# Optimization experiments

Measured on AMD Instinct MI355X. Metric: run time of the kernel, lower is better.

The kernel has to match this reference:

```python
import jax, jax.numpy as jnp
import numpy as np

FEAT_DIM = 384
HEAD_DIM = 32
N_HEADS = FEAT_DIM // HEAD_DIM
MAX_SEQ_LEN = 64
SIZE = 8  # sqrt(max_seq_len)


def _get_relative_position_index(height, width):
    coords_h = np.arange(height)
    coords_w = np.arange(width)
    coords = np.stack(np.meshgrid(coords_h, coords_w, indexing='ij'))
    coords_flat = coords.reshape(coords.shape[0], -1)
    relative_coords = coords_flat[:, :, None] - coords_flat[:, None, :]
    relative_coords = relative_coords.transpose(1, 2, 0)
    rh = relative_coords[:, :, 0] + (height - 1)
    rw = relative_coords[:, :, 1] + (width - 1)
    return jnp.asarray(rh * (2 * width - 1) + rw, dtype=jnp.int32)  # [P, P]


def setup_inputs() -> dict:
    key = jax.random.key(0)
    ks = jax.random.split(key, 6)
    B, G, P, D = 32, 64, MAX_SEQ_LEN, FEAT_DIM
    x = jax.random.normal(ks[0], (B, G, P, D), dtype=jnp.float32)
    qkv_w = jax.random.normal(ks[1], (D, 3 * D), dtype=jnp.float32) * (1.0 / np.sqrt(D))
    qkv_b = jnp.zeros((3 * D,), dtype=jnp.float32)
    merge_w = jax.random.normal(ks[2], (D, D), dtype=jnp.float32) * (1.0 / np.sqrt(D))
    merge_b = jnp.zeros((D,), dtype=jnp.float32)
    n_bias = (2 * SIZE - 1) * (2 * SIZE - 1)  # 225
    bias_table = jax.random.truncated_normal(ks[3], -2.0, 2.0, (n_bias, N_HEADS), dtype=jnp.float32) * 0.02
    rel_index = _get_relative_position_index(SIZE, SIZE)
    return {"x": x, "qkv_w": qkv_w, "qkv_b": qkv_b, "merge_w": merge_w,
            "merge_b": merge_b, "bias_table": bias_table, "rel_index": rel_index}


def reference(x, qkv_w, qkv_b, merge_w, merge_b, bias_table, rel_index):
    B, G, P, D = x.shape
    H, DH = N_HEADS, HEAD_DIM
    scale = 1.0 / np.sqrt(D)  # NOTE: module scales by feat_dim**-0.5, not head_dim
    qkv = x @ qkv_w + qkv_b  # [B,G,P,3D]
    q, k, v = jnp.split(qkv, 3, axis=-1)
    q = q.reshape(B, G, P, H, DH).transpose(0, 1, 3, 2, 4)  # [B,G,H,P,DH]
    k = k.reshape(B, G, P, H, DH).transpose(0, 1, 3, 2, 4)
    v = v.reshape(B, G, P, H, DH).transpose(0, 1, 3, 2, 4)
    scores = jnp.einsum('bghid,bghjd->bghij', q, k * scale)  # [B,G,H,P,P]
    pos_bias = bias_table[rel_index.reshape(-1)].reshape(P, P, H)
    pos_bias = pos_bias.transpose(2, 0, 1)[None, None]  # [1,1,H,P,P]
    attn = jax.nn.softmax(scores + pos_bias, axis=-1)
    out = jnp.einsum('bghij,bghjd->bghid', attn, v)  # [B,G,H,P,DH]
    out = out.transpose(0, 1, 3, 2, 4).reshape(B, G, P, D)
    return out @ merge_w + merge_b
```

## Files before the change

kernel.cpp:

```cpp
#include <hip/hip_runtime.h>
#include <hip/hip_bf16.h>
#include <cstdint>
#include <cstddef>


typedef __bf16 bf16_t;
typedef __bf16 bf16x8 __attribute__((ext_vector_type(8)));
typedef float  f32x4  __attribute__((ext_vector_type(4)));

#define MFMA16(A, B, C) __builtin_amdgcn_mfma_f32_16x16x32_bf16((A), (B), (C), 0, 0, 0)

#define SCALE  0.051031036307982884f
#define LOG2E  1.4426950408889634f

#define BAR()  do { asm volatile("s_waitcnt lgkmcnt(0)" ::: "memory"); \
                    __builtin_amdgcn_s_barrier(); } while (0)


__global__ void prep_kernel(const float* __restrict__ qkv_w,
                            const float* __restrict__ qkv_b,
                            const float* __restrict__ merge_w,
                            const float* __restrict__ bias_table,
                            const int*   __restrict__ rel_index,
                            bf16_t* __restrict__ qkv_wT,
                            bf16_t* __restrict__ merge_wT,
                            bf16_t* __restrict__ biasx,
                            float*  __restrict__ qkvb_s) {
  int idx = blockIdx.x * 256 + threadIdx.x;
  if (idx < 1152 * 384) {
    int n = idx / 384, k = idx - n * 384;
    float v = qkv_w[k * 1152 + n];
    if (n >= 384 && n < 768) v *= SCALE;
    qkv_wT[idx] = (bf16_t)v;
    return;
  }
  int i2 = idx - 1152 * 384;
  if (i2 < 384 * 384) {
    int n = i2 / 384, k = i2 - n * 384;
    merge_wT[i2] = (bf16_t)merge_w[k * 384 + n];
    return;
  }
  int i3 = i2 - 384 * 384;
  if (i3 < 12 * 64 * 64) {
    int h = i3 / 4096, r = i3 - h * 4096;
    biasx[i3] = (bf16_t)bias_table[rel_index[r] * 12 + h];
    return;
  }
  int i4 = i3 - 12 * 64 * 64;
  if (i4 < 1152) {
    float v = qkv_b[i4];
    if (i4 >= 384 && i4 < 768) v *= SCALE;
    qkvb_s[i4] = v;
  }
}

__device__ inline float bflo(unsigned u) {
  union { unsigned x; float f; } v; v.x = u << 16; return v.f;
}
__device__ inline float bfhi(unsigned u) {
  union { unsigned x; float f; } v; v.x = u & 0xffff0000u; return v.f;
}

__global__ void __launch_bounds__(768, 6)
fused_qkv_attn(const float*  __restrict__ x,
               const bf16_t* __restrict__ wT,
               const float*  __restrict__ qbias,
               const bf16_t* __restrict__ biasx,
               bf16_t* __restrict__ attn) {
  extern __shared__ char smem_raw[];
  bf16_t* lds = (bf16_t*)smem_raw;
  bf16_t* xs  = lds;
  bf16_t* qs  = lds;
  bf16_t* ks  = lds + 8192;
  bf16_t* vts = lds + 16384;
  bf16_t* ps  = lds + 24576;

  const int tid  = threadIdx.x;
  const int lane = tid & 63;
  const int w    = tid >> 6;
  const int c    = lane & 15;
  const int g    = lane >> 4;
  const int cx   = c & 7;

  const int xcd  = blockIdx.x & 7;
  const int slot = blockIdx.x >> 3;
  const int pass = slot % 3;
  const int bg   = (slot / 3) * 8 + xcd;

  const f32x4 zf = {0.f, 0.f, 0.f, 0.f};

  {
    const float4* xg = (const float4*)(x + (size_t)bg * 24576);
#pragma unroll
    for (int it = 0; it < 4; ++it) {
      int hc  = tid + it * 768;
      int row = hc / 48;
      int ch  = hc - row * 48;
      float4 v0 = xg[hc * 2];
      float4 v1 = xg[hc * 2 + 1];
      union { bf16_t b[8]; bf16x8 v; } pk;
      pk.b[0] = (bf16_t)v0.x; pk.b[1] = (bf16_t)v0.y;
      pk.b[2] = (bf16_t)v0.z; pk.b[3] = (bf16_t)v0.w;
      pk.b[4] = (bf16_t)v1.x; pk.b[5] = (bf16_t)v1.y;
      pk.b[6] = (bf16_t)v1.z; pk.b[7] = (bf16_t)v1.w;
      *(bf16x8*)(xs + row * 384 + ((ch ^ (row & 7)) << 3)) = pk.v;
    }
  }
  BAR();

  f32x4 acc[2][4];
#pragma unroll
  for (int t = 0; t < 2; ++t)
#pragma unroll
    for (int mt = 0; mt < 4; ++mt) acc[t][mt] = zf;

  int nrow[2];
  const int kind = (w * 2) >> 3;
  int hlv[2], c16v[2];
  const bf16_t* wp[2];
  float bv[2];
#pragma unroll
  for (int t = 0; t < 2; ++t) {
    int tau  = w * 2 + t;
    int u    = tau & 7;
    hlv[t]   = u >> 1;
    c16v[t]  = u & 1;
    nrow[t]  = kind * 384 + (pass * 4 + hlv[t]) * 32 + c16v[t] * 16;
    wp[t]    = wT + (size_t)(nrow[t] + c) * 384 + g * 8;
    bv[t]    = qbias[nrow[t] + c];
  }
  bf16x8 bc[2], bn[2];
#pragma unroll
  for (int t = 0; t < 2; ++t) bc[t] = *(const bf16x8*)(wp[t]);

#pragma unroll
  for (int k = 0; k < 12; ++k) {
    if (k < 11) {
#pragma unroll
      for (int t = 0; t < 2; ++t) bn[t] = *(const bf16x8*)(wp[t] + (k + 1) * 32);
    }
    int chv = (((4 * k + g) ^ cx) << 3);
#pragma unroll
    for (int mt = 0; mt < 4; ++mt) {
      bf16x8 a = *(const bf16x8*)(xs + (mt * 16 + c) * 384 + chv);
#pragma unroll
      for (int t = 0; t < 2; ++t)
        acc[t][mt] = MFMA16(a, bc[t], acc[t][mt]);
    }
#pragma unroll
    for (int t = 0; t < 2; ++t) bc[t] = bn[t];
  }

  BAR();

#pragma unroll
  for (int t = 0; t < 2; ++t) {
    int hl = hlv[t], c16 = c16v[t];
    if (kind == 2) {
      int d = c16 * 16 + c;
      bf16_t* vbase = vts + hl * 2048 + d * 64;
#pragma unroll
      for (int mt = 0; mt < 4; ++mt) {
        union { bf16_t b[4]; uint2 u2; } pk;
#pragma unroll
        for (int r = 0; r < 4; ++r) pk.b[r] = (bf16_t)(acc[t][mt][r] + bv[t]);
        int chunk = (2 * mt + (g >> 1)) ^ cx;
        *(uint2*)(vbase + chunk * 8 + (g & 1) * 4) = pk.u2;
      }
    } else {
      int f  = c16 * 16 + c;
      int fc = f >> 3;
      int fl = f & 7;
      bf16_t* dst = (kind == 0 ? qs : ks) + hl * 2048;
#pragma unroll
      for (int mt = 0; mt < 4; ++mt)
#pragma unroll
        for (int r = 0; r < 4; ++r)
          dst[(mt * 16 + g * 4 + r) * 32 + ((fc ^ g) << 3) + fl] =
              (bf16_t)(acc[t][mt][r] + bv[t]);
    }
  }
  BAR();

  if (w < 8) {
    const int hl = w >> 1, ih = w & 1;
    const int h  = pass * 4 + hl;
    const int rsw = (c >> 2) & 3;

    const bf16_t* bp = biasx + h * 4096;
    bf16x8 ka[4], va[2][2];
#pragma unroll
    for (int mt = 0; mt < 4; ++mt)
      ka[mt] = *(const bf16x8*)(ks + hl * 2048 + (mt * 16 + c) * 32 +
                                ((g ^ rsw) << 3));
#pragma unroll
    for (int m2 = 0; m2 < 2; ++m2)
#pragma unroll
      for (int kt = 0; kt < 2; ++kt)
        va[m2][kt] = *(const bf16x8*)(vts + hl * 2048 + (m2 * 16 + c) * 64 +
                                      (((4 * kt + g) ^ cx) << 3));

    bf16_t* psw = ps + w * 1024;

#pragma unroll
    for (int nt = 0; nt < 2; ++nt) {
      int i = ih * 32 + nt * 16 + c;
      bf16x8 qf = *(const bf16x8*)(qs + hl * 2048 + i * 32 + ((g ^ rsw) << 3));

      f32x4 sacc[4];
#pragma unroll
      for (int mt = 0; mt < 4; ++mt) sacc[mt] = zf;
#pragma unroll
      for (int mt = 0; mt < 4; ++mt)
        sacc[mt] = MFMA16(ka[mt], qf, sacc[mt]);

      float l = 0.f;
#pragma unroll
      for (int mt = 0; mt < 4; ++mt) {
        uint2 bb = *(const uint2*)(bp + i * 64 + mt * 16 + g * 4);
        float p0 = exp2f((sacc[mt][0] + bflo(bb.x)) * LOG2E);
        float p1 = exp2f((sacc[mt][1] + bfhi(bb.x)) * LOG2E);
        float p2 = exp2f((sacc[mt][2] + bflo(bb.y)) * LOG2E);
        float p3 = exp2f((sacc[mt][3] + bfhi(bb.y)) * LOG2E);
        l += (p0 + p1) + (p2 + p3);
        union { bf16_t b[4]; uint2 u2; } pk;
        pk.b[0] = (bf16_t)p0; pk.b[1] = (bf16_t)p1;
        pk.b[2] = (bf16_t)p2; pk.b[3] = (bf16_t)p3;
        int chunk = (2 * mt + (g >> 1)) ^ cx;
        *(uint2*)(psw + c * 64 + chunk * 8 + (g & 1) * 4) = pk.u2;
      }
      bf16x8 pb[2];
#pragma unroll
      for (int kt = 0; kt < 2; ++kt)
        pb[kt] = *(const bf16x8*)(psw + c * 64 + (((4 * kt + g) ^ cx) << 3));
      f32x4 oacc[2];
#pragma unroll
      for (int m2 = 0; m2 < 2; ++m2) oacc[m2] = zf;
#pragma unroll
      for (int m2 = 0; m2 < 2; ++m2)
#pragma unroll
        for (int kt = 0; kt < 2; ++kt)
          oacc[m2] = MFMA16(va[m2][kt], pb[kt], oacc[m2]);

      l += __shfl_xor(l, 16);
      l += __shfl_xor(l, 32);
      float inv = 1.0f / l;

      int row = bg * 64 + i;
#pragma unroll
      for (int m2 = 0; m2 < 2; ++m2) {
        union { bf16_t b[4]; uint2 u2; } pk;
#pragma unroll
        for (int r = 0; r < 4; ++r) pk.b[r] = (bf16_t)(oacc[m2][r] * inv);
        *(uint2*)(attn + (size_t)row * 384 + h * 32 + m2 * 16 + g * 4) = pk.u2;
      }
    }
  }
}

#define XS 408
__global__ void __launch_bounds__(512)
merge_gemm(const bf16_t* __restrict__ attn,
           const bf16_t* __restrict__ mwT,
           const float*  __restrict__ mb,
           float* __restrict__ out) {
  __shared__ bf16_t as[64 * XS];
  const int tid = threadIdx.x, blk = blockIdx.x;
  const int lane = tid & 63, w = tid >> 6, c = lane & 15, g = lane >> 4;

  {
    const int4* ag = (const int4*)(attn + (size_t)blk * (64 * 384));
#pragma unroll
    for (int it = 0; it < 6; ++it) {
      int idx = tid + it * 512;
      int row = idx / 48;
      int col = (idx - row * 48) * 8;
      *(int4*)(as + row * XS + col) = ag[idx];
    }
  }
  __syncthreads();

  const f32x4 zf = {0.f, 0.f, 0.f, 0.f};
  f32x4 acc[3][4];
#pragma unroll
  for (int t = 0; t < 3; ++t)
#pragma unroll
    for (int mt = 0; mt < 4; ++mt) acc[t][mt] = zf;

  const int n0 = w * 48;
  const bf16_t* wp[3];
#pragma unroll
  for (int t = 0; t < 3; ++t) wp[t] = mwT + (size_t)(n0 + t * 16 + c) * 384 + g * 8;
  bf16x8 bc[3], bn[3];
#pragma unroll
  for (int t = 0; t < 3; ++t) bc[t] = *(const bf16x8*)(wp[t]);
#pragma unroll
  for (int k = 0; k < 12; ++k) {
    if (k < 11) {
#pragma unroll
      for (int t = 0; t < 3; ++t) bn[t] = *(const bf16x8*)(wp[t] + (k + 1) * 32);
    }
    bf16x8 a[4];
#pragma unroll
    for (int mt = 0; mt < 4; ++mt)
      a[mt] = *(const bf16x8*)(as + (mt * 16 + c) * XS + k * 32 + g * 8);
#pragma unroll
    for (int t = 0; t < 3; ++t)
#pragma unroll
      for (int mt = 0; mt < 4; ++mt)
        acc[t][mt] = MFMA16(a[mt], bc[t], acc[t][mt]);
#pragma unroll
    for (int t = 0; t < 3; ++t) bc[t] = bn[t];
  }

#pragma unroll
  for (int t = 0; t < 3; ++t) {
    float bias = mb[n0 + t * 16 + c];
#pragma unroll
    for (int mt = 0; mt < 4; ++mt)
#pragma unroll
      for (int r = 0; r < 4; ++r)
        out[(size_t)(blk * 64 + mt * 16 + g * 4 + r) * 384 + n0 + t * 16 + c] =
            acc[t][mt][r] + bias;
  }
}

extern "C" void kernel_launch(void* const* d_in, const int* in_sizes, int n_in,
                              void* d_out, int out_size, void* d_ws, size_t ws_size,
                              hipStream_t stream) {
  const float* x          = (const float*)d_in[0];
  const float* qkv_w      = (const float*)d_in[1];
  const float* qkv_b      = (const float*)d_in[2];
  const float* merge_w    = (const float*)d_in[3];
  const float* merge_b    = (const float*)d_in[4];
  const float* bias_table = (const float*)d_in[5];
  const int*   rel_index  = (const int*)d_in[6];
  float*       out        = (float*)d_out;

  const size_t OFF_QKVWT = 0;
  const size_t OFF_MWT   = 884736;
  const size_t OFF_BIAS  = OFF_MWT + 294912;
  const size_t OFF_QB    = OFF_BIAS + 98304;
  const size_t OFF_ATTN  = OFF_QB + 4608;
  const size_t NEED      = OFF_ATTN + (size_t)100663296;
  if (ws_size < NEED) return;

  char* ws = (char*)d_ws;
  bf16_t* qkv_wT  = (bf16_t*)(ws + OFF_QKVWT);
  bf16_t* mwT     = (bf16_t*)(ws + OFF_MWT);
  bf16_t* biasx   = (bf16_t*)(ws + OFF_BIAS);
  float*  qkvb_s  = (float*)(ws + OFF_QB);
  bf16_t* attnbuf = (bf16_t*)(ws + OFF_ATTN);

  prep_kernel<<<2501, 256, 0, stream>>>(qkv_w, qkv_b, merge_w, bias_table,
                                        rel_index, qkv_wT, mwT, biasx, qkvb_s);

  hipFuncSetAttribute(reinterpret_cast<const void*>(fused_qkv_attn),
                      hipFuncAttributeMaxDynamicSharedMemorySize, 65536);
  fused_qkv_attn<<<6144, 768, 65536, stream>>>(x, qkv_wT, qkvb_s, biasx, attnbuf);

  merge_gemm<<<2048, 512, 0, stream>>>(attnbuf, mwT, merge_b, out);
}
```

Baseline: 409.1 us.

## Fuse QKV, attention, and merge projection into one kernel per group

Result: slower. 677.2 us (+65.5%).

```diff
diff --git a/kernel.cpp b/kernel.cpp
--- a/kernel.cpp
+++ b/kernel.cpp
@@ -62,18 +62,21 @@
 }
 
 __global__ void __launch_bounds__(768, 6)
-fused_qkv_attn(const float*  __restrict__ x,
-               const bf16_t* __restrict__ wT,
-               const float*  __restrict__ qbias,
-               const bf16_t* __restrict__ biasx,
-               bf16_t* __restrict__ attn) {
+mega_kernel(const float*  __restrict__ x,
+            const bf16_t* __restrict__ wT,
+            const float*  __restrict__ qbias,
+            const bf16_t* __restrict__ biasx,
+            const bf16_t* __restrict__ mwT,
+            const float*  __restrict__ mb,
+            float* __restrict__ out) {
   extern __shared__ char smem_raw[];
   bf16_t* lds = (bf16_t*)smem_raw;
   bf16_t* xs  = lds;
-  bf16_t* qs  = lds;
-  bf16_t* ks  = lds + 8192;
-  bf16_t* vts = lds + 16384;
-  bf16_t* ps  = lds + 24576;
+  bf16_t* qs  = lds + 24576;
+  bf16_t* ks  = lds + 32768;
+  bf16_t* vts = lds + 40960;
+  bf16_t* ao  = lds + 49152;
+  bf16_t* ps  = qs;
 
   const int tid  = threadIdx.x;
   const int lane = tid & 63;
@@ -81,11 +84,7 @@
   const int c    = lane & 15;
   const int g    = lane >> 4;
   const int cx   = c & 7;
-
-  const int xcd  = blockIdx.x & 7;
-  const int slot = blockIdx.x >> 3;
-  const int pass = slot % 3;
-  const int bg   = (slot / 3) * 8 + xcd;
+  const int bg   = blockIdx.x;
 
   const f32x4 zf = {0.f, 0.f, 0.f, 0.f};
 
@@ -108,220 +107,210 @@
   }
   BAR();
 
-  f32x4 acc[2][4];
-#pragma unroll
-  for (int t = 0; t < 2; ++t)
-#pragma unroll
-    for (int mt = 0; mt < 4; ++mt) acc[t][mt] = zf;
-
-  int nrow[2];
-  const int kind = (w * 2) >> 3;
-  int hlv[2], c16v[2];
-  const bf16_t* wp[2];
-  float bv[2];
-#pragma unroll
-  for (int t = 0; t < 2; ++t) {
-    int tau  = w * 2 + t;
-    int u    = tau & 7;
-    hlv[t]   = u >> 1;
-    c16v[t]  = u & 1;
-    nrow[t]  = kind * 384 + (pass * 4 + hlv[t]) * 32 + c16v[t] * 16;
-    wp[t]    = wT + (size_t)(nrow[t] + c) * 384 + g * 8;
-    bv[t]    = qbias[nrow[t] + c];
-  }
-  bf16x8 bc[2], bn[2];
-#pragma unroll
-  for (int t = 0; t < 2; ++t) bc[t] = *(const bf16x8*)(wp[t]);
-
-#pragma unroll
-  for (int k = 0; k < 12; ++k) {
-    if (k < 11) {
-#pragma unroll
-      for (int t = 0; t < 2; ++t) bn[t] = *(const bf16x8*)(wp[t] + (k + 1) * 32);
-    }
-    int chv = (((4 * k + g) ^ cx) << 3);
-#pragma unroll
-    for (int mt = 0; mt < 4; ++mt) {
-      bf16x8 a = *(const bf16x8*)(xs + (mt * 16 + c) * 384 + chv);
-#pragma unroll
-      for (int t = 0; t < 2; ++t)
-        acc[t][mt] = MFMA16(a, bc[t], acc[t][mt]);
-    }
-#pragma unroll
-    for (int t = 0; t < 2; ++t) bc[t] = bn[t];
-  }
-
-  BAR();
-
-#pragma unroll
-  for (int t = 0; t < 2; ++t) {
-    int hl = hlv[t], c16 = c16v[t];
-    if (kind == 2) {
-      int d = c16 * 16 + c;
-      bf16_t* vbase = vts + hl * 2048 + d * 64;
+#pragma unroll 1
+  for (int pass = 0; pass < 3; ++pass) {
+    f32x4 acc[2][4];
+#pragma unroll
+    for (int t = 0; t < 2; ++t)
+#pragma unroll
+      for (int mt = 0; mt < 4; ++mt) acc[t][mt] = zf;
+
+    const int kind = (w * 2) >> 3;
+    int nrow[2], hlv[2], c16v[2];
+    const bf16_t* wp[2];
+    float bv[2];
+#pragma unroll
+    for (int t = 0; t < 2; ++t) {
+      int tau  = w * 2 + t;
+      int u    = tau & 7;
+      hlv[t]   = u >> 1;
+      c16v[t]  = u & 1;
+      nrow[t]  = kind * 384 + (pass * 4 + hlv[t]) * 32 + c16v[t] * 16;
+      wp[t]    = wT + (size_t)(nrow[t] + c) * 384 + g * 8;
+      bv[t]    = qbias[nrow[t] + c];
+    }
+    bf16x8 bc[2], bn[2];
+#pragma unroll
+    for (int t = 0; t < 2; ++t) bc[t] = *(const bf16x8*)(wp[t]);
+
+#pragma unroll
+    for (int k = 0; k < 12; ++k) {
+      if (k < 11) {
+#pragma unroll
+        for (int t = 0; t < 2; ++t) bn[t] = *(const bf16x8*)(wp[t] + (k + 1) * 32);
+      }
+      int chv = (((4 * k + g) ^ cx) << 3);
 #pragma unroll
       for (int mt = 0; mt < 4; ++mt) {
-        union { bf16_t b[4]; uint2 u2; } pk;
-#pragma unroll
-        for (int r = 0; r < 4; ++r) pk.b[r] = (bf16_t)(acc[t][mt][r] + bv[t]);
-        int chunk = (2 * mt + (g >> 1)) ^ cx;
-        *(uint2*)(vbase + chunk * 8 + (g & 1) * 4) = pk.u2;
-      }
-    } else {
-      int f  = c16 * 16 + c;
-      int fc = f >> 3;
-      int fl = f & 7;
-      bf16_t* dst = (kind == 0 ? qs : ks) + hl * 2048;
-#pragma unroll
-      for (int mt = 0; mt < 4; ++mt)
-#pragma unroll
-        for (int r = 0; r < 4; ++r)
-          dst[(mt * 16 + g * 4 + r) * 32 + ((fc ^ g) << 3) + fl] =
-              (bf16_t)(acc[t][mt][r] + bv[t]);
-    }
-  }
-  BAR();
-
-  if (w < 8) {
+        bf16x8 a = *(const bf16x8*)(xs + (mt * 16 + c) * 384 + chv);
+#pragma unroll
+        for (int t = 0; t < 2; ++t)
+          acc[t][mt] = MFMA16(a, bc[t], acc[t][mt]);
+      }
+#pragma unroll
+      for (int t = 0; t < 2; ++t) bc[t] = bn[t];
+    }
+
+    BAR();
+
+#pragma unroll
+    for (int t = 0; t < 2; ++t) {
+      int hl = hlv[t], c16 = c16v[t];
+      if (kind == 2) {
+        int d = c16 * 16 + c;
+        bf16_t* vbase = vts + hl * 2048 + d * 64;
+#pragma unroll
+        for (int mt = 0; mt < 4; ++mt) {
+          union { bf16_t b[4]; uint2 u2; } pk;
+#pragma unroll
+          for (int r = 0; r < 4; ++r) pk.b[r] = (bf16_t)(acc[t][mt][r] + bv[t]);
+          int chunk = (2 * mt + (g >> 1)) ^ cx;
+          *(uint2*)(vbase + chunk * 8 + (g & 1) * 4) = pk.u2;
+        }
+      } else {
+        int f  = c16 * 16 + c;
+        int fc = f >> 3;
+        int fl = f & 7;
+        bf16_t* dst = (kind == 0 ? qs : ks) + hl * 2048;
+#pragma unroll
+        for (int mt = 0; mt < 4; ++mt)
+#pragma unroll
+          for (int r = 0; r < 4; ++r)
+            dst[(mt * 16 + g * 4 + r) * 32 + ((fc ^ g) << 3) + fl] =
+                (bf16_t)(acc[t][mt][r] + bv[t]);
+      }
+    }
+    BAR();
+
     const int hl = w >> 1, ih = w & 1;
     const int h  = pass * 4 + hl;
     const int rsw = (c >> 2) & 3;
-
-    const bf16_t* bp = biasx + h * 4096;
-    bf16x8 ka[4], va[2][2];
-#pragma unroll
-    for (int mt = 0; mt < 4; ++mt)
-      ka[mt] = *(const bf16x8*)(ks + hl * 2048 + (mt * 16 + c) * 32 +
-                                ((g ^ rsw) << 3));
-#pragma unroll
-    for (int m2 = 0; m2 < 2; ++m2)
-#pragma unroll
-      for (int kt = 0; kt < 2; ++kt)
-        va[m2][kt] = *(const bf16x8*)(vts + hl * 2048 + (m2 * 16 + c) * 64 +
-                                      (((4 * kt + g) ^ cx) << 3));
-
-    bf16_t* psw = ps + w * 1024;
-
-#pragma unroll
-    for (int nt = 0; nt < 2; ++nt) {
-      int i = ih * 32 + nt * 16 + c;
-      bf16x8 qf = *(const bf16x8*)(qs + hl * 2048 + i * 32 + ((g ^ rsw) << 3));
-
-      f32x4 sacc[4];
-#pragma unroll
-      for (int mt = 0; mt < 4; ++mt) sacc[mt] = zf;
+    bf16x8 ka[4], qf[2], va[2][2];
+    if (w < 8) {
 #pragma unroll
       for (int mt = 0; mt < 4; ++mt)
-        sacc[mt] = MFMA16(ka[mt], qf, sacc[mt]);
-
-      float l = 0.f;
+        ka[mt] = *(const bf16x8*)(ks + hl * 2048 + (mt * 16 + c) * 32 +
+                                  ((g ^ rsw) << 3));
+#pragma unroll
+      for (int nt = 0; nt < 2; ++nt)
+        qf[nt] = *(const bf16x8*)(qs + hl * 2048 +
+                                  (ih * 32 + nt * 16 + c) * 32 + ((g ^ rsw) << 3));
+#pragma unroll
+      for (int m2 = 0; m2 < 2; ++m2)
+#pragma unroll
+        for (int kt = 0; kt < 2; ++kt)
+          va[m2][kt] = *(const bf16x8*)(vts + hl * 2048 + (m2 * 16 + c) * 64 +
+                                        (((4 * kt + g) ^ cx) << 3));
+    }
+    BAR();
+
+    if (w < 8) {
+      const bf16_t* bp = biasx + h * 4096;
+      bf16_t* psw = ps + w * 1024;
+
+#pragma unroll
+      for (int nt = 0; nt < 2; ++nt) {
+        int i = ih * 32 + nt * 16 + c;
+
+        f32x4 sacc[4];
+#pragma unroll
+        for (int mt = 0; mt < 4; ++mt) sacc[mt] = zf;
+#pragma unroll
+        for (int mt = 0; mt < 4; ++mt)
+          sacc[mt] = MFMA16(ka[mt], qf[nt], sacc[mt]);
+
+        float l = 0.f;
+#pragma unroll
+        for (int mt = 0; mt < 4; ++mt) {
+          uint2 bb = *(const uint2*)(bp + i * 64 + mt * 16 + g * 4);
+          float p0 = exp2f((sacc[mt][0] + bflo(bb.x)) * LOG2E);
+          float p1 = exp2f((sacc[mt][1] + bfhi(bb.x)) * LOG2E);
+          float p2 = exp2f((sacc[mt][2] + bflo(bb.y)) * LOG2E);
+          float p3 = exp2f((sacc[mt][3] + bfhi(bb.y)) * LOG2E);
+          l += (p0 + p1) + (p2 + p3);
+          union { bf16_t b[4]; uint2 u2; } pk;
+          pk.b[0] = (bf16_t)p0; pk.b[1] = (bf16_t)p1;
+          pk.b[2] = (bf16_t)p2; pk.b[3] = (bf16_t)p3;
+          int chunk = (2 * mt + (g >> 1)) ^ cx;
+          *(uint2*)(psw + c * 64 + chunk * 8 + (g & 1) * 4) = pk.u2;
+        }
+        bf16x8 pb[2];
+#pragma unroll
+        for (int kt = 0; kt < 2; ++kt)
+          pb[kt] = *(const bf16x8*)(psw + c * 64 + (((4 * kt + g) ^ cx) << 3));
+        f32x4 oacc[2];
+#pragma unroll
+        for (int m2 = 0; m2 < 2; ++m2) oacc[m2] = zf;
+#pragma unroll
+        for (int m2 = 0; m2 < 2; ++m2)
+#pragma unroll
+          for (int kt = 0; kt < 2; ++kt)
+            oacc[m2] = MFMA16(va[m2][kt], pb[kt], oacc[m2]);
+
+        l += __shfl_xor(l, 16);
+        l += __shfl_xor(l, 32);
+        float inv = 1.0f / l;
+
+#pragma unroll
+        for (int m2 = 0; m2 < 2; ++m2) {
+          union { bf16_t b[4]; uint2 u2; } pk;
+#pragma unroll
+          for (int r = 0; r < 4; ++r) pk.b[r] = (bf16_t)(oacc[m2][r] * inv);
+          int ch = (h * 32 + m2 * 16 + g * 4) >> 3;
+          *(uint2*)(ao + i * 384 + ((ch ^ (i & 7)) << 3) + (g & 1) * 4) = pk.u2;
+        }
+      }
+    }
+  }
+
+  BAR();
+
+  {
+    f32x4 acc[2][4];
+#pragma unroll
+    for (int t = 0; t < 2; ++t)
+#pragma unroll
+      for (int mt = 0; mt < 4; ++mt) acc[t][mt] = zf;
+
+    int n0[2];
+    const bf16_t* wp[2];
+    float mbv[2];
+#pragma unroll
+    for (int t = 0; t < 2; ++t) {
+      n0[t] = (w * 2 + t) * 16;
+      wp[t] = mwT + (size_t)(n0[t] + c) * 384 + g * 8;
+      mbv[t] = mb[n0[t] + c];
+    }
+    bf16x8 bc[2], bn[2];
+#pragma unroll
+    for (int t = 0; t < 2; ++t) bc[t] = *(const bf16x8*)(wp[t]);
+
+#pragma unroll
+    for (int k = 0; k < 12; ++k) {
+      if (k < 11) {
+#pragma unroll
+        for (int t = 0; t < 2; ++t) bn[t] = *(const bf16x8*)(wp[t] + (k + 1) * 32);
+      }
+      int chv = (((4 * k + g) ^ cx) << 3);
 #pragma unroll
       for (int mt = 0; mt < 4; ++mt) {
-        uint2 bb = *(const uint2*)(bp + i * 64 + mt * 16 + g * 4);
-        float p0 = exp2f((sacc[mt][0] + bflo(bb.x)) * LOG2E);
-        float p1 = exp2f((sacc[mt][1] + bfhi(bb.x)) * LOG2E);
-        float p2 = exp2f((sacc[mt][2] + bflo(bb.y)) * LOG2E);
-        float p3 = exp2f((sacc[mt][3] + bfhi(bb.y)) * LOG2E);
-        l += (p0 + p1) + (p2 + p3);
-        union { bf16_t b[4]; uint2 u2; } pk;
-        pk.b[0] = (bf16_t)p0; pk.b[1] = (bf16_t)p1;
-        pk.b[2] = (bf16_t)p2; pk.b[3] = (bf16_t)p3;
-        int chunk = (2 * mt + (g >> 1)) ^ cx;
-        *(uint2*)(psw + c * 64 + chunk * 8 + (g & 1) * 4) = pk.u2;
-      }
-      bf16x8 pb[2];
-#pragma unroll
-      for (int kt = 0; kt < 2; ++kt)
-        pb[kt] = *(const bf16x8*)(psw + c * 64 + (((4 * kt + g) ^ cx) << 3));
-      f32x4 oacc[2];
-#pragma unroll
-      for (int m2 = 0; m2 < 2; ++m2) oacc[m2] = zf;
-#pragma unroll
-      for (int m2 = 0; m2 < 2; ++m2)
-#pragma unroll
-        for (int kt = 0; kt < 2; ++kt)
-          oacc[m2] = MFMA16(va[m2][kt], pb[kt], oacc[m2]);
-
-      l += __shfl_xor(l, 16);
-      l += __shfl_xor(l, 32);
-      float inv = 1.0f / l;
-
-      int row = bg * 64 + i;
-#pragma unroll
-      for (int m2 = 0; m2 < 2; ++m2) {
-        union { bf16_t b[4]; uint2 u2; } pk;
-#pragma unroll
-        for (int r = 0; r < 4; ++r) pk.b[r] = (bf16_t)(oacc[m2][r] * inv);
-        *(uint2*)(attn + (size_t)row * 384 + h * 32 + m2 * 16 + g * 4) = pk.u2;
-      }
-    }
-  }
-}
-
-#define XS 408
-__global__ void __launch_bounds__(512)
-merge_gemm(const bf16_t* __restrict__ attn,
-           const bf16_t* __restrict__ mwT,
-           const float*  __restrict__ mb,
-           float* __restrict__ out) {
-  __shared__ bf16_t as[64 * XS];
-  const int tid = threadIdx.x, blk = blockIdx.x;
-  const int lane = tid & 63, w = tid >> 6, c = lane & 15, g = lane >> 4;
-
-  {
-    const int4* ag = (const int4*)(attn + (size_t)blk * (64 * 384));
-#pragma unroll
-    for (int it = 0; it < 6; ++it) {
-      int idx = tid + it * 512;
-      int row = idx / 48;
-      int col = (idx - row * 48) * 8;
-      *(int4*)(as + row * XS + col) = ag[idx];
-    }
-  }
-  __syncthreads();
-
-  const f32x4 zf = {0.f, 0.f, 0.f, 0.f};
-  f32x4 acc[3][4];
-#pragma unroll
-  for (int t = 0; t < 3; ++t)
-#pragma unroll
-    for (int mt = 0; mt < 4; ++mt) acc[t][mt] = zf;
-
-  const int n0 = w * 48;
-  const bf16_t* wp[3];
-#pragma unroll
-  for (int t = 0; t < 3; ++t) wp[t] = mwT + (size_t)(n0 + t * 16 + c) * 384 + g * 8;
-  bf16x8 bc[3], bn[3];
-#pragma unroll
-  for (int t = 0; t < 3; ++t) bc[t] = *(const bf16x8*)(wp[t]);
-#pragma unroll
-  for (int k = 0; k < 12; ++k) {
-    if (k < 11) {
-#pragma unroll
-      for (int t = 0; t < 3; ++t) bn[t] = *(const bf16x8*)(wp[t] + (k + 1) * 32);
-    }
-    bf16x8 a[4];
-#pragma unroll
-    for (int mt = 0; mt < 4; ++mt)
-      a[mt] = *(const bf16x8*)(as + (mt * 16 + c) * XS + k * 32 + g * 8);
-#pragma unroll
-    for (int t = 0; t < 3; ++t)
+        bf16x8 a = *(const bf16x8*)(ao + (mt * 16 + c) * 384 + chv);
+#pragma unroll
+        for (int t = 0; t < 2; ++t)
+          acc[t][mt] = MFMA16(a, bc[t], acc[t][mt]);
+      }
+#pragma unroll
+      for (int t = 0; t < 2; ++t) bc[t] = bn[t];
+    }
+
+#pragma unroll
+    for (int t = 0; t < 2; ++t)
 #pragma unroll
       for (int mt = 0; mt < 4; ++mt)
-        acc[t][mt] = MFMA16(a[mt], bc[t], acc[t][mt]);
-#pragma unroll
-    for (int t = 0; t < 3; ++t) bc[t] = bn[t];
-  }
-
-#pragma unroll
-  for (int t = 0; t < 3; ++t) {
-    float bias = mb[n0 + t * 16 + c];
-#pragma unroll
-    for (int mt = 0; mt < 4; ++mt)
-#pragma unroll
-      for (int r = 0; r < 4; ++r)
-        out[(size_t)(blk * 64 + mt * 16 + g * 4 + r) * 384 + n0 + t * 16 + c] =
-            acc[t][mt][r] + bias;
+#pragma unroll
+        for (int r = 0; r < 4; ++r)
+          out[(size_t)(bg * 64 + mt * 16 + g * 4 + r) * 384 + n0[t] + c] =
+              acc[t][mt][r] + mbv[t];
   }
 }
 
@@ -341,8 +330,7 @@
   const size_t OFF_MWT   = 884736;
   const size_t OFF_BIAS  = OFF_MWT + 294912;
   const size_t OFF_QB    = OFF_BIAS + 98304;
-  const size_t OFF_ATTN  = OFF_QB + 4608;
-  const size_t NEED      = OFF_ATTN + (size_t)100663296;
+  const size_t NEED      = OFF_QB + 4608;
   if (ws_size < NEED) return;
 
   char* ws = (char*)d_ws;
@@ -350,14 +338,12 @@
   bf16_t* mwT     = (bf16_t*)(ws + OFF_MWT);
   bf16_t* biasx   = (bf16_t*)(ws + OFF_BIAS);
   float*  qkvb_s  = (float*)(ws + OFF_QB);
-  bf16_t* attnbuf = (bf16_t*)(ws + OFF_ATTN);
 
   prep_kernel<<<2501, 256, 0, stream>>>(qkv_w, qkv_b, merge_w, bias_table,
                                         rel_index, qkv_wT, mwT, biasx, qkvb_s);
 
-  hipFuncSetAttribute(reinterpret_cast<const void*>(fused_qkv_attn),
-                      hipFuncAttributeMaxDynamicSharedMemorySize, 65536);
-  fused_qkv_attn<<<6144, 768, 65536, stream>>>(x, qkv_wT, qkvb_s, biasx, attnbuf);
-
-  merge_gemm<<<2048, 512, 0, stream>>>(attnbuf, mwT, merge_b, out);
-}
+  hipFuncSetAttribute(reinterpret_cast<const void*>(mega_kernel),
+                      hipFuncAttributeMaxDynamicSharedMemorySize, 147456);
+  mega_kernel<<<2048, 768, 147456, stream>>>(x, qkv_wT, qkvb_s, biasx, mwT,
+                                             merge_b, out);
+}
```
